# Optimization experiments

Hardware: AMD Instinct MI355X
Metric: run time of the kernel (lower is better)

## Reference

```python
import jax, jax.numpy as jnp
import numpy as np

B, N, C, H = 4, 1024, 768, 12
D = C // H
HID = 4 * C
SCALE = D ** -0.5
EPS = 1e-6


def layernorm(x, w, b):
    mu = jnp.mean(x, axis=-1, keepdims=True)
    var = jnp.mean(jnp.square(x - mu), axis=-1, keepdims=True)
    return (x - mu) * jax.lax.rsqrt(var + EPS) * w + b


def setup_inputs() -> dict:
    key = jax.random.key(0)
    ks = jax.random.split(key, 16)
    s = lambda fan_in: 1.0 / np.sqrt(fan_in)
    return {
        "x": jax.random.normal(ks[0], (B, N, C), jnp.float32),
        "physics_bias": jax.random.normal(ks[1], (B, N, N), jnp.float32),
        "qkv_w": jax.random.normal(ks[2], (C, 3 * C), jnp.float32) * s(C),
        "qkv_b": jnp.zeros((3 * C,), jnp.float32),
        "proj_w": jax.random.normal(ks[3], (C, C), jnp.float32) * s(C),
        "proj_b": jnp.zeros((C,), jnp.float32),
        "n1_w": jnp.ones((C,), jnp.float32),
        "n1_b": jnp.zeros((C,), jnp.float32),
        "n2_w": jnp.ones((C,), jnp.float32),
        "n2_b": jnp.zeros((C,), jnp.float32),
        "fc1_w": jax.random.normal(ks[4], (C, HID), jnp.float32) * s(C),
        "fc1_b": jnp.zeros((HID,), jnp.float32),
        "fc2_w": jax.random.normal(ks[5], (HID, C), jnp.float32) * s(HID),
        "fc2_b": jnp.zeros((C,), jnp.float32),
    }


def reference(x, physics_bias, qkv_w, qkv_b, proj_w, proj_b,
              n1_w, n1_b, n2_w, n2_b, fc1_w, fc1_b, fc2_w, fc2_b):
    # --- biased self-attention (pre-norm) ---
    h = layernorm(x, n1_w, n1_b)                         # [B,N,C]
    qkv = (h @ qkv_w + qkv_b).reshape(B, N, 3, H, D)     # [B,N,3,H,D]
    q, k, v = (qkv[:, :, i] for i in range(3))           # each [B,N,H,D]
    attn = jnp.einsum('bnhd,bmhd->bhnm', q, k) * SCALE   # [B,H,N,N]
    attn = attn + physics_bias[:, None, :, :]            # additive physics bias
    attn = jax.nn.softmax(attn, axis=-1)
    o = jnp.einsum('bhnm,bmhd->bnhd', attn, v).reshape(B, N, C)
    x = x + (o @ proj_w + proj_b)
    # --- MLP (pre-norm) ---
    h = layernorm(x, n2_w, n2_b)
    h = jax.nn.gelu(h @ fc1_w + fc1_b, approximate=False)
    x = x + (h @ fc2_w + fc2_b)
    return x
```

## Files before the change

### kernel.cpp

```cpp
#include <hip/hip_runtime.h>
#include <hip/hip_bf16.h>
#include <cstdint>
#include <cstddef>

#define B_   4
#define N_   1024
#define C_   768
#define H_   12
#define D_   64
#define HID_ 3072
#define M_   4096

typedef __attribute__((ext_vector_type(8))) short short8;
typedef __attribute__((ext_vector_type(8))) unsigned short ushort8;
typedef __attribute__((ext_vector_type(4))) float f32x4;

__device__ __forceinline__ void gload16(const void* g, void* l) {
  __builtin_amdgcn_global_load_lds(
      (const __attribute__((address_space(1))) void*)g,
      (__attribute__((address_space(3))) void*)l, 16, 0, 0);
}

__device__ __forceinline__ unsigned short f2bf(float f) {
  __hip_bfloat16 h = __float2bfloat16(f);
  return __builtin_bit_cast(unsigned short, h);
}
__device__ __forceinline__ float bf2f(unsigned short u) {
  unsigned int x = ((unsigned int)u) << 16;
  return __builtin_bit_cast(float, x);
}
__device__ __forceinline__ float ex2(float x) {
  float r;
  asm("v_exp_f32 %0, %1" : "=v"(r) : "v"(x));
  return r;
}
__device__ __forceinline__ float frcp(float x) {
  float r;
  asm("v_rcp_f32 %0, %1" : "=v"(r) : "v"(x));
  return r;
}

__global__ __launch_bounds__(256) void wconv_all(
    const float* __restrict__ qkv_w, const float* __restrict__ proj_w,
    const float* __restrict__ fc1_w, const float* __restrict__ fc2_w,
    unsigned short* __restrict__ wt_qkv, unsigned short* __restrict__ wt_proj,
    unsigned short* __restrict__ wt_fc1, unsigned short* __restrict__ wt_fc2) {
  __shared__ float tile[32][33];
  const int bid = blockIdx.x;
  const float* W;
  unsigned short* Wt;
  int K, Nn, bx, by;
  if (bid < 1728) {
    W = qkv_w; Wt = wt_qkv; K = 768; Nn = 2304;
    bx = bid % 72; by = bid / 72;
  } else if (bid < 1728 + 576) {
    const int i = bid - 1728;
    W = proj_w; Wt = wt_proj; K = 768; Nn = 768;
    bx = i % 24; by = i / 24;
  } else if (bid < 1728 + 576 + 2304) {
    const int i = bid - (1728 + 576);
    W = fc1_w; Wt = wt_fc1; K = 768; Nn = 3072;
    bx = i % 96; by = i / 96;
  } else {
    const int i = bid - (1728 + 576 + 2304);
    W = fc2_w; Wt = wt_fc2; K = 3072; Nn = 768;
    bx = i % 24; by = i / 24;
  }
  const int tx = threadIdx.x & 31, ty = threadIdx.x >> 5;
  const int n0 = bx * 32, k0 = by * 32;
#pragma unroll
  for (int i = 0; i < 32; i += 8)
    tile[ty + i][tx] = W[(size_t)(k0 + ty + i) * Nn + n0 + tx];
  __syncthreads();
#pragma unroll
  for (int i = 0; i < 32; i += 8)
    Wt[(size_t)(n0 + ty + i) * K + k0 + tx] = f2bf(tile[tx][ty + i]);
}

__global__ __launch_bounds__(256) void ln_kernel(const float* __restrict__ x,
                                                 const float* __restrict__ w,
                                                 const float* __restrict__ b,
                                                 unsigned short* __restrict__ out) {
  __shared__ float sbuf[8];
  const int row = blockIdx.x;
  const int t = threadIdx.x;
  const float* xr = x + (size_t)row * C_;
  float v0 = xr[t], v1 = xr[t + 256], v2 = xr[t + 512];
  float s = v0 + v1 + v2;
  float ss = v0 * v0 + v1 * v1 + v2 * v2;
#pragma unroll
  for (int m = 32; m >= 1; m >>= 1) {
    s += __shfl_xor(s, m);
    ss += __shfl_xor(ss, m);
  }
  const int wave = t >> 6, lane = t & 63;
  if (lane == 0) { sbuf[wave] = s; sbuf[4 + wave] = ss; }
  __syncthreads();
  s = sbuf[0] + sbuf[1] + sbuf[2] + sbuf[3];
  ss = sbuf[4] + sbuf[5] + sbuf[6] + sbuf[7];
  const float mu = s * (1.f / C_);
  const float var = ss * (1.f / C_) - mu * mu;
  const float rstd = rsqrtf(var + 1e-6f);
  unsigned short* o = out + (size_t)row * C_;
  o[t]       = f2bf((v0 - mu) * rstd * w[t]       + b[t]);
  o[t + 256] = f2bf((v1 - mu) * rstd * w[t + 256] + b[t + 256]);
  o[t + 512] = f2bf((v2 - mu) * rstd * w[t + 512] + b[t + 512]);
}

template <int MF, bool GELU, bool RES, bool OUTF, bool OUTB>
__global__ __launch_bounds__(256) void gemm_bt(const unsigned short* __restrict__ A,
                                               const unsigned short* __restrict__ Bt,
                                               const float* __restrict__ bias,
                                               const float* __restrict__ res,
                                               float* __restrict__ outF,
                                               unsigned short* __restrict__ outB,
                                               int M, int Nn, int K) {
  __shared__ unsigned short As[5][MF * 32 * 32];
  __shared__ unsigned short Bs[5][128 * 32];
  const int t = threadIdx.x;
  const int lane = t & 63;
  const int wave = t >> 6;
  const int wm = wave >> 1, wn = wave & 1;
  const int r15 = lane & 15, g = lane >> 4;

  constexpr int SPX = (MF == 4) ? 4 : 8;
  constexpr int LGS = (MF == 4) ? 2 : 3;
  const int orig = blockIdx.y * gridDim.x + blockIdx.x;
  const int xcd = orig & 7;
  const int j = orig >> 3;
  const int bm = xcd * SPX + (j & (SPX - 1));
  const int bn = j >> LGS;

  f32x4 acc[MF][4];
#pragma unroll
  for (int m = 0; m < MF; ++m)
#pragma unroll
    for (int n = 0; n < 4; ++n) acc[m][n] = (f32x4){0.f, 0.f, 0.f, 0.f};

  const unsigned short* ga0 = A + (size_t)(bm * (MF * 32) + (t >> 2)) * K + (t & 3) * 8;
  const unsigned short* gb0 = Bt + (size_t)(bn * 128 + (t >> 2)) * K + (t & 3) * 8;

#define GSTAGE(kt_, buf_)                                                  \
  {                                                                        \
    const unsigned short* ga = ga0 + (kt_)*32;                             \
    const unsigned short* gb = gb0 + (kt_)*32;                             \
    gload16(ga, (char*)As[buf_] + wave * 1024);                            \
    if constexpr (MF == 4)                                                 \
      gload16(ga + (size_t)64 * K, (char*)As[buf_] + wave * 1024 + 4096);  \
    gload16(gb, (char*)Bs[buf_] + wave * 1024);                            \
    gload16(gb + (size_t)64 * K, (char*)Bs[buf_] + wave * 1024 + 4096);    \
  }

  const int nk = K >> 5;
  GSTAGE(0, 0);
  GSTAGE(1, 1);
  GSTAGE(2, 2);
  GSTAGE(3, 3);

  int rd = 0;
  for (int kt = 0; kt < nk; ++kt) {
    const int rem = nk - kt;
    if (rem >= 4) {
      if constexpr (MF == 4) asm volatile("s_waitcnt vmcnt(12)" ::: "memory");
      else                   asm volatile("s_waitcnt vmcnt(9)" ::: "memory");
    } else if (rem == 3) {
      if constexpr (MF == 4) asm volatile("s_waitcnt vmcnt(8)" ::: "memory");
      else                   asm volatile("s_waitcnt vmcnt(6)" ::: "memory");
    } else if (rem == 2) {
      if constexpr (MF == 4) asm volatile("s_waitcnt vmcnt(4)" ::: "memory");
      else                   asm volatile("s_waitcnt vmcnt(3)" ::: "memory");
    } else {
      asm volatile("s_waitcnt vmcnt(0)" ::: "memory");
    }
    __builtin_amdgcn_s_barrier();

    short8 af[MF], bf[4];
#pragma unroll
    for (int m = 0; m < MF; ++m)
      af[m] = *(const short8*)(As[rd] + (wm * (MF * 16) + m * 16 + r15) * 32 + g * 8);
#pragma unroll
    for (int n = 0; n < 4; ++n)
      bf[n] = *(const short8*)(Bs[rd] + (wn * 64 + n * 16 + r15) * 32 + g * 8);

    if (kt + 4 < nk) {
      const int wr = (rd == 0) ? 4 : rd - 1;
      GSTAGE(kt + 4, wr);
    }

    asm volatile("s_waitcnt lgkmcnt(0)" ::: "memory");
    __builtin_amdgcn_sched_barrier(0);
    __builtin_amdgcn_s_setprio(1);
#pragma unroll
    for (int m = 0; m < MF; ++m)
#pragma unroll
      for (int n = 0; n < 4; ++n)
        acc[m][n] = __builtin_amdgcn_mfma_f32_16x16x32_bf16(af[m], bf[n], acc[m][n], 0, 0, 0);
    __builtin_amdgcn_s_setprio(0);
    rd = (rd == 4) ? 0 : rd + 1;
  }
#undef GSTAGE

#pragma unroll
  for (int m = 0; m < MF; ++m) {
#pragma unroll
    for (int n = 0; n < 4; ++n) {
#pragma unroll
      for (int r = 0; r < 4; ++r) {
        const int row = bm * (MF * 32) + wm * (MF * 16) + m * 16 + g * 4 + r;
        const int col = bn * 128 + wn * 64 + n * 16 + r15;
        float v = acc[m][n][r] + bias[col];
        if (GELU) v = 0.5f * v * (1.f + erff(v * 0.70710678118654752f));
        if (RES) v += res[(size_t)row * Nn + col];
        if (OUTF) outF[(size_t)row * Nn + col] = v;
        if (OUTB) outB[(size_t)row * Nn + col] = f2bf(v);
      }
    }
  }
}

__global__ __launch_bounds__(256) void attn_kernel(const unsigned short* __restrict__ qkv,
                                                   const float* __restrict__ pbias,
                                                   unsigned short* __restrict__ o) {
  __shared__ unsigned short Ks[2][64 * 64];
  __shared__ unsigned short Vt[64 * 64];
  __shared__ unsigned short Ps[4][16 * 64];
  const int t = threadIdx.x, lane = t & 63, wave = t >> 6;
  const int bh = blockIdx.y;
  const int b = bh / H_, h = bh % H_;
  const int q0 = blockIdx.x * 64;
  const int r15 = lane & 15, g = lane >> 4;
  const int qrow = q0 + wave * 16;
  const float LOG2E = 1.44269504088896f;
  const float QS = 0.125f * 1.44269504088896f;
  const int NT = N_ / 64;

  short8 aq[2];
  {
    const unsigned short* qp =
        qkv + (size_t)(b * N_ + qrow + r15) * (3 * C_) + h * D_ + g * 8;
    const ushort8 r0 = *(const ushort8*)qp;
    const ushort8 r1 = *(const ushort8*)(qp + 32);
#pragma unroll
    for (int jj = 0; jj < 8; ++jj) {
      aq[0][jj] = (short)f2bf(bf2f(r0[jj]) * QS);
      aq[1][jj] = (short)f2bf(bf2f(r1[jj]) * QS);
    }
  }
  short8 ones;
#pragma unroll
  for (int jj = 0; jj < 8; ++jj) ones[jj] = (short)0x3F80;

  f32x4 oacc[4], lacc;
#pragma unroll
  for (int n = 0; n < 4; ++n) oacc[n] = (f32x4){0.f, 0.f, 0.f, 0.f};
  lacc = (f32x4){0.f, 0.f, 0.f, 0.f};
  float m_run[4];
#pragma unroll
  for (int r = 0; r < 4; ++r) m_run[r] = -1e30f;

  const unsigned short* kbase = qkv + (size_t)b * N_ * (3 * C_) + C_ + h * D_;
  const unsigned short* vbase = qkv + (size_t)b * N_ * (3 * C_) + 2 * C_ + h * D_;

  const float* bp[4];
#pragma unroll
  for (int r = 0; r < 4; ++r)
    bp[r] = pbias + (size_t)b * N_ * N_ + (size_t)(qrow + g * 4 + r) * N_ + r15;

  const int krow = t >> 3;
  const int kchunk = (t & 7) ^ (krow & 7);
  const int vp = t & 31;
  const int vq = t >> 5;
  const int vkey = vp * 2, vd0 = vq * 8;

#define KSTAGE(kb_, nb_)                                                       \
  {                                                                            \
    const unsigned short* kg =                                                 \
        kbase + (size_t)((kb_)*64 + krow) * (3 * C_) + kchunk * 8;             \
    gload16(kg, (char*)Ks[nb_] + wave * 1024);                                 \
    gload16(kg + (size_t)32 * (3 * C_), (char*)Ks[nb_] + wave * 1024 + 4096);  \
  }

#define VWRITE(va_, vb_)                                                             \
  {                                                                                  \
    char* vdst = (char*)Vt;                                                          \
    _Pragma("unroll") for (int jj = 0; jj < 8; ++jj) {                               \
      const int d = vd0 + jj;                                                        \
      const unsigned int pack =                                                      \
          (unsigned int)(va_)[jj] | ((unsigned int)(vb_)[jj] << 16);                 \
      *(unsigned int*)(vdst + d * 128 + (((vp >> 2) ^ (d & 7)) << 4) +               \
                       (vp & 3) * 4) = pack;                                         \
    }                                                                                \
  }

  KSTAGE(0, 0);
  ushort8 va, vb2;
  {
    const unsigned short* vg = vbase + (size_t)vkey * (3 * C_) + vd0;
    va = *(const ushort8*)vg;
    vb2 = *(const ushort8*)(vg + 3 * C_);
  }
  float bcur[4][4], bnext[4][4];
#pragma unroll
  for (int n = 0; n < 4; ++n)
#pragma unroll
    for (int r = 0; r < 4; ++r) bcur[n][r] = bp[r][n * 16];

  for (int kb = 0; kb < NT; ++kb) {
    const int cur = kb & 1;
    __syncthreads();

    VWRITE(va, vb2);

    const bool more = (kb + 1 < NT);
    if (more) {
      KSTAGE(kb + 1, cur ^ 1);
      const unsigned short* vg =
          vbase + (size_t)((kb + 1) * 64 + vkey) * (3 * C_) + vd0;
      va = *(const ushort8*)vg;
      vb2 = *(const ushort8*)(vg + 3 * C_);
#pragma unroll
      for (int n = 0; n < 4; ++n)
#pragma unroll
        for (int r = 0; r < 4; ++r) bnext[n][r] = bp[r][64 + n * 16];
    }
#pragma unroll
    for (int r = 0; r < 4; ++r) bp[r] += 64;

    const unsigned short* Ksc = Ks[cur];
    f32x4 sacc[4];
#pragma unroll
    for (int n = 0; n < 4; ++n) sacc[n] = (f32x4){0.f, 0.f, 0.f, 0.f};
    __builtin_amdgcn_s_setprio(1);
#pragma unroll
    for (int kk = 0; kk < 2; ++kk) {
#pragma unroll
      for (int n = 0; n < 4; ++n) {
        short8 bk = *(const short8*)(Ksc + (n * 16 + r15) * 64 +
                                     (((kk * 4 + g) ^ (r15 & 7)) << 3));
        sacc[n] = __builtin_amdgcn_mfma_f32_16x16x32_bf16(aq[kk], bk, sacc[n], 0, 0, 0);
      }
    }
    __builtin_amdgcn_s_setprio(0);

    float p[4][4], tm[4];
#pragma unroll
    for (int n = 0; n < 4; ++n)
#pragma unroll
      for (int r = 0; r < 4; ++r)
        p[n][r] = fmaf(bcur[n][r], LOG2E, sacc[n][r]);
#pragma unroll
    for (int r = 0; r < 4; ++r)
      tm[r] = fmaxf(fmaxf(p[0][r], p[1][r]), fmaxf(p[2][r], p[3][r]));
#pragma unroll
    for (int r = 0; r < 4; ++r) {
      tm[r] = fmaxf(tm[r], __shfl_xor(tm[r], 1));
      tm[r] = fmaxf(tm[r], __shfl_xor(tm[r], 2));
      tm[r] = fmaxf(tm[r], __shfl_xor(tm[r], 4));
      tm[r] = fmaxf(tm[r], __shfl_xor(tm[r], 8));
    }
    int need = 0;
#pragma unroll
    for (int r = 0; r < 4; ++r) need |= (tm[r] > m_run[r] + 8.0f);
    if (__any(need)) {
#pragma unroll
      for (int r = 0; r < 4; ++r) {
        const float mn = fmaxf(m_run[r], tm[r]);
        const float corr = ex2(m_run[r] - mn);
        m_run[r] = mn;
        lacc[r] *= corr;
#pragma unroll
        for (int n = 0; n < 4; ++n) oacc[n][r] *= corr;
      }
    }
#pragma unroll
    for (int n = 0; n < 4; ++n)
#pragma unroll
      for (int r = 0; r < 4; ++r) p[n][r] = ex2(p[n][r] - m_run[r]);

    unsigned short* Psw = Ps[wave];
#pragma unroll
    for (int n = 0; n < 4; ++n)
#pragma unroll
      for (int r = 0; r < 4; ++r) {
        const int row = g * 4 + r, col = n * 16 + r15;
        Psw[row * 64 + (((col >> 3) ^ (row & 7)) << 3) + (col & 7)] = f2bf(p[n][r]);
      }

    asm volatile("s_waitcnt lgkmcnt(0)" ::: "memory");
    __builtin_amdgcn_s_barrier();
    __builtin_amdgcn_sched_barrier(0);

    __builtin_amdgcn_s_setprio(1);
#pragma unroll
    for (int kk = 0; kk < 2; ++kk) {
      short8 ap = *(const short8*)(Psw + r15 * 64 + (((kk * 4 + g) ^ (r15 & 7)) << 3));
      lacc = __builtin_amdgcn_mfma_f32_16x16x32_bf16(ap, ones, lacc, 0, 0, 0);
#pragma unroll
      for (int n = 0; n < 4; ++n) {
        short8 bv = *(const short8*)(Vt + (n * 16 + r15) * 64 +
                                     (((kk * 4 + g) ^ (r15 & 7)) << 3));
        oacc[n] = __builtin_amdgcn_mfma_f32_16x16x32_bf16(ap, bv, oacc[n], 0, 0, 0);
      }
    }
    __builtin_amdgcn_s_setprio(0);

    if (more) {
#pragma unroll
      for (int n = 0; n < 4; ++n)
#pragma unroll
        for (int r = 0; r < 4; ++r) bcur[n][r] = bnext[n][r];
    }
  }
#undef KSTAGE
#undef VWRITE

  float rl[4];
#pragma unroll
  for (int r = 0; r < 4; ++r) rl[r] = frcp(lacc[r]);
#pragma unroll
  for (int n = 0; n < 4; ++n) {
#pragma unroll
    for (int r = 0; r < 4; ++r) {
      const int row = qrow + g * 4 + r;
      const float v = oacc[n][r] * rl[r];
      o[(size_t)(b * N_ + row) * C_ + h * D_ + n * 16 + r15] = f2bf(v);
    }
  }
}

extern "C" void kernel_launch(void* const* d_in, const int* in_sizes, int n_in,
                              void* d_out, int out_size, void* d_ws, size_t ws_size,
                              hipStream_t stream) {
  const float* x      = (const float*)d_in[0];
  const float* pbias  = (const float*)d_in[1];
  const float* qkv_w  = (const float*)d_in[2];
  const float* qkv_b  = (const float*)d_in[3];
  const float* proj_w = (const float*)d_in[4];
  const float* proj_b = (const float*)d_in[5];
  const float* n1_w   = (const float*)d_in[6];
  const float* n1_b   = (const float*)d_in[7];
  const float* n2_w   = (const float*)d_in[8];
  const float* n2_b   = (const float*)d_in[9];
  const float* fc1_w  = (const float*)d_in[10];
  const float* fc1_b  = (const float*)d_in[11];
  const float* fc2_w  = (const float*)d_in[12];
  const float* fc2_b  = (const float*)d_in[13];
  float* out = (float*)d_out;

  char* ws = (char*)d_ws;
  unsigned short* wt_qkv  = (unsigned short*)(ws + 0);
  unsigned short* wt_proj = (unsigned short*)(ws + 3538944);
  unsigned short* wt_fc1  = (unsigned short*)(ws + 4718592);
  unsigned short* wt_fc2  = (unsigned short*)(ws + 9437184);
  float*          x2      = (float*)(ws + 14155776);
  unsigned short* h1      = (unsigned short*)(ws + 26738688);
  unsigned short* qkvb    = (unsigned short*)(ws + 33030144);

  wconv_all<<<1728 + 576 + 2304 + 2304, 256, 0, stream>>>(
      qkv_w, proj_w, fc1_w, fc2_w, wt_qkv, wt_proj, wt_fc1, wt_fc2);

  ln_kernel<<<M_, 256, 0, stream>>>(x, n1_w, n1_b, h1);
  gemm_bt<4, false, false, false, true><<<dim3(32, 18), 256, 0, stream>>>(
      h1, wt_qkv, qkv_b, nullptr, nullptr, qkvb, M_, 3 * C_, C_);
  attn_kernel<<<dim3(N_ / 64, B_ * H_), 256, 0, stream>>>(qkvb, pbias, h1);
  gemm_bt<2, false, true, true, false><<<dim3(64, 6), 256, 0, stream>>>(
      h1, wt_proj, proj_b, x, x2, nullptr, M_, C_, C_);
  ln_kernel<<<M_, 256, 0, stream>>>(x2, n2_w, n2_b, h1);
  gemm_bt<4, true, false, false, true><<<dim3(32, 24), 256, 0, stream>>>(
      h1, wt_fc1, fc1_b, nullptr, nullptr, qkvb, M_, HID_, C_);
  gemm_bt<2, false, true, true, false><<<dim3(64, 6), 256, 0, stream>>>(
      qkvb, wt_fc2, fc2_b, x2, out, nullptr, M_, C_, HID_);
}
```

Measured before the change: 199.0 us.

## Swizzle GEMM LDS tiles and shrink pipeline from 5 to 3 stages

```diff
diff --git a/kernel.cpp b/kernel.cpp
--- a/kernel.cpp
+++ b/kernel.cpp
@@ -115,8 +115,8 @@
                                                float* __restrict__ outF,
                                                unsigned short* __restrict__ outB,
                                                int M, int Nn, int K) {
-  __shared__ unsigned short As[5][MF * 32 * 32];
-  __shared__ unsigned short Bs[5][128 * 32];
+  __shared__ unsigned short As[3][MF * 32 * 32];
+  __shared__ unsigned short Bs[3][128 * 32];
   const int t = threadIdx.x;
   const int lane = t & 63;
   const int wave = t >> 6;
@@ -137,8 +137,10 @@
 #pragma unroll
     for (int n = 0; n < 4; ++n) acc[m][n] = (f32x4){0.f, 0.f, 0.f, 0.f};
 
-  const unsigned short* ga0 = A + (size_t)(bm * (MF * 32) + (t >> 2)) * K + (t & 3) * 8;
-  const unsigned short* gb0 = Bt + (size_t)(bn * 128 + (t >> 2)) * K + (t & 3) * 8;
+  const int srow = t >> 2;
+  const int schunk = (t & 3) ^ ((t >> 3) & 3);
+  const unsigned short* ga0 = A + (size_t)(bm * (MF * 32) + srow) * K + schunk * 8;
+  const unsigned short* gb0 = Bt + (size_t)(bn * 128 + srow) * K + schunk * 8;
 
 #define GSTAGE(kt_, buf_)                                                  \
   {                                                                        \
@@ -154,19 +156,23 @@
   const int nk = K >> 5;
   GSTAGE(0, 0);
   GSTAGE(1, 1);
-  GSTAGE(2, 2);
-  GSTAGE(3, 3);
+
+  int arow[MF], aoff[MF], boff[4];
+#pragma unroll
+  for (int m = 0; m < MF; ++m) {
+    arow[m] = wm * (MF * 16) + m * 16 + r15;
+    aoff[m] = arow[m] * 32 + (g ^ ((arow[m] >> 1) & 3)) * 8;
+  }
+#pragma unroll
+  for (int n = 0; n < 4; ++n) {
+    const int rn = wn * 64 + n * 16 + r15;
+    boff[n] = rn * 32 + (g ^ ((rn >> 1) & 3)) * 8;
+  }
 
   int rd = 0;
   for (int kt = 0; kt < nk; ++kt) {
     const int rem = nk - kt;
-    if (rem >= 4) {
-      if constexpr (MF == 4) asm volatile("s_waitcnt vmcnt(12)" ::: "memory");
-      else                   asm volatile("s_waitcnt vmcnt(9)" ::: "memory");
-    } else if (rem == 3) {
-      if constexpr (MF == 4) asm volatile("s_waitcnt vmcnt(8)" ::: "memory");
-      else                   asm volatile("s_waitcnt vmcnt(6)" ::: "memory");
-    } else if (rem == 2) {
+    if (rem >= 2) {
       if constexpr (MF == 4) asm volatile("s_waitcnt vmcnt(4)" ::: "memory");
       else                   asm volatile("s_waitcnt vmcnt(3)" ::: "memory");
     } else {
@@ -177,14 +183,14 @@
     short8 af[MF], bf[4];
 #pragma unroll
     for (int m = 0; m < MF; ++m)
-      af[m] = *(const short8*)(As[rd] + (wm * (MF * 16) + m * 16 + r15) * 32 + g * 8);
+      af[m] = *(const short8*)(As[rd] + aoff[m]);
 #pragma unroll
     for (int n = 0; n < 4; ++n)
-      bf[n] = *(const short8*)(Bs[rd] + (wn * 64 + n * 16 + r15) * 32 + g * 8);
-
-    if (kt + 4 < nk) {
-      const int wr = (rd == 0) ? 4 : rd - 1;
-      GSTAGE(kt + 4, wr);
+      bf[n] = *(const short8*)(Bs[rd] + boff[n]);
+
+    if (kt + 2 < nk) {
+      const int wr = (rd + 2 >= 3) ? rd - 1 : rd + 2;
+      GSTAGE(kt + 2, wr);
     }
 
     asm volatile("s_waitcnt lgkmcnt(0)" ::: "memory");
@@ -196,7 +202,7 @@
       for (int n = 0; n < 4; ++n)
         acc[m][n] = __builtin_amdgcn_mfma_f32_16x16x32_bf16(af[m], bf[n], acc[m][n], 0, 0, 0);
     __builtin_amdgcn_s_setprio(0);
-    rd = (rd == 4) ? 0 : rd + 1;
+    rd = (rd == 2) ? 0 : rd + 1;
   }
 #undef GSTAGE
 
```

New measurement: 178.2 us. 10.5% less time.
